# Kernel optimization log

Hardware: AMD Instinct MI355X
Metric: run time of the kernel (lower is better)

## Reference

```python
import jax, jax.numpy as jnp
import numpy as np
from jax import lax

C_IN, C_OUT, K = 32, 32, 3
DIV = float(np.sqrt(C_IN * K * K))  # sqrt(channels_in * filter_size^2)


def setup_inputs() -> dict:
    key = jax.random.key(0)
    kx, kw = jax.random.split(key)
    x = jax.random.normal(kx, (32, C_IN, 256, 256), dtype=jnp.float32)  # NCHW
    # torch.normal(0.0, 0.01, (Cout, Cin, k, k))
    weight = 0.01 * jax.random.normal(kw, (C_OUT, C_IN, K, K), dtype=jnp.float32)
    return {"x": x, "weight": weight}


def reference(x, weight):
    # binarize weights: sign with 0 -> -1 (torch.where(x > 0, 1.0, -1.0))
    weight_bin = jnp.where(weight > 0, 1.0, -1.0).astype(weight.dtype)
    # conv2d with 'same' padding (padding = k // 2, stride 1)
    out = lax.conv_general_dilated(
        x, weight_bin,
        window_strides=(1, 1),
        padding=((K // 2, K // 2), (K // 2, K // 2)),
        dimension_numbers=("NCHW", "OIHW", "NCHW"),
    )
    return out / DIV
```

## Files before the change

### kernel.cpp

```cpp
#include <hip/hip_runtime.h>


typedef __attribute__((ext_vector_type(8))) short short8;
typedef __attribute__((ext_vector_type(4))) float f32x4;

__device__ __forceinline__ unsigned short f2bf(float f) {
    unsigned int u = __builtin_bit_cast(unsigned int, f);
    u += 0x7FFFu + ((u >> 16) & 1u);
    return (unsigned short)(u >> 16);
}

__device__ __forceinline__ int lds_idx(int s, int p, int u) {
    return s * 264 + p * 4 + (u ^ ((p >> 1) & 3));
}

__global__ __launch_bounds__(512, 4)
void bconv2d_kernel(const float* __restrict__ x, const float* __restrict__ wgt,
                    float* __restrict__ out) {
    __shared__ short8 lds[8 * 264];

    const int tid = threadIdx.x;
    const int gx0 = blockIdx.x * 64;
    const int Y0  = blockIdx.y * 64;
    const int n   = blockIdx.z;

    const int l      = tid & 63;
    const int wv     = tid >> 6;
    const int r      = wv & 3;
    const int ch     = wv >> 2;
    const int lane15 = l & 15;
    const int lhi    = l >> 4;

    short8 afrag[3][3];
    {
        const int co  = ch * 16 + lane15;
        const int ci0 = lhi * 8;
        #pragma unroll
        for (int dy = 0; dy < 3; ++dy) {
            #pragma unroll
            for (int dx = 0; dx < 3; ++dx) {
                short8 a;
                #pragma unroll
                for (int j = 0; j < 8; ++j) {
                    float wval = wgt[((co * 32 + (ci0 + j)) * 3 + dy) * 3 + dx];
                    a[j] = (short)((wval > 0.0f) ? 0x3F80 : 0xBF80);
                }
                afrag[dy][dx] = a;
            }
        }
    }

    auto stage = [&](int gy0v, int nrows) {
        const int ntask = nrows * 264;
        for (int task = tid; task < ntask; task += 512) {
            const int row = task / 264;
            const int rem = task - row * 264;
            const int u   = rem / 66;
            const int p   = rem - u * 66;
            const int gy  = gy0v + row;
            const int gx  = gx0 - 1 + p;
            short8 v = (short8)0;
            if ((unsigned)gy < 256u && (unsigned)gx < 256u) {
                const float* src = x + (((size_t)n * 32 + u * 8) * 256 + gy) * 256 + gx;
                #pragma unroll
                for (int j = 0; j < 8; ++j)
                    v[j] = (short)f2bf(src[(size_t)j * 65536]);
            }
            lds[lds_idx(gy & 7, p, u)] = v;
        }
    };

    stage(Y0 - 1, 6);
    __syncthreads();

    const float invdiv = 0.05892556509887896f;

    for (int i = 0; i < 16; ++i) {
        const int Y = Y0 + 4 * i;
        const int y = Y + r;

        f32x4 acc[4];
        #pragma unroll
        for (int tp = 0; tp < 4; ++tp) acc[tp] = (f32x4)0.0f;

        #pragma unroll
        for (int dy = 0; dy < 3; ++dy) {
            const int sbase = ((y - 1 + dy) & 7) * 264;
            #pragma unroll
            for (int dx = 0; dx < 3; ++dx) {
                #pragma unroll
                for (int tp = 0; tp < 4; ++tp) {
                    const int p = tp * 16 + lane15 + dx;
                    short8 b = lds[sbase + p * 4 + (lhi ^ ((p >> 1) & 3))];
                    acc[tp] = __builtin_amdgcn_mfma_f32_16x16x32_bf16(
                        afrag[dy][dx], b, acc[tp], 0, 0, 0);
                }
            }
        }

        #pragma unroll
        for (int tp = 0; tp < 4; ++tp) {
            #pragma unroll
            for (int rr = 0; rr < 4; ++rr) {
                const int co = ch * 16 + lhi * 4 + rr;
                out[(((size_t)n * 32 + co) * 256 + y) * 256 + gx0 + tp * 16 + lane15]
                    = acc[tp][rr] * invdiv;
            }
        }

        __syncthreads();
        if (i < 15) stage(Y + 5, 4);
        __syncthreads();
    }
}

extern "C" void kernel_launch(void* const* d_in, const int* in_sizes, int n_in,
                              void* d_out, int out_size, void* d_ws, size_t ws_size,
                              hipStream_t stream) {
    const float* x   = (const float*)d_in[0];
    const float* wgt = (const float*)d_in[1];
    float* out = (float*)d_out;
    dim3 grid(4, 4, 32);
    dim3 block(512);
    bconv2d_kernel<<<grid, block, 0, stream>>>(x, wgt, out);
}
```

Baseline: 139.3 us.

## Split rows into 8-row blocks with two-row register blocking per wave

Each block now handles 8 output rows instead of 64, so the grid grows eightfold. Each block stages a 10-row halo once and no longer runs a sliding-window loop with per-iteration barriers. Each wave computes two adjacent output rows and reuses each LDS B fragment for both rows' MFMAs. The cost is a larger halo re-read (10 rows loaded per 8 outputs instead of 66 per 64) and a higher occupancy target in the launch bounds.

After: 305.8 us. 120% more time.

```diff
diff --git a/kernel.cpp b/kernel.cpp
--- a/kernel.cpp
+++ b/kernel.cpp
@@ -10,23 +10,19 @@
     return (unsigned short)(u >> 16);
 }
 
-__device__ __forceinline__ int lds_idx(int s, int p, int u) {
-    return s * 264 + p * 4 + (u ^ ((p >> 1) & 3));
-}
-
-__global__ __launch_bounds__(512, 4)
+__global__ __launch_bounds__(512, 6)
 void bconv2d_kernel(const float* __restrict__ x, const float* __restrict__ wgt,
                     float* __restrict__ out) {
-    __shared__ short8 lds[8 * 264];
+    __shared__ short8 lds[10 * 264];
 
     const int tid = threadIdx.x;
     const int gx0 = blockIdx.x * 64;
-    const int Y0  = blockIdx.y * 64;
+    const int Y0  = blockIdx.y * 8;
     const int n   = blockIdx.z;
 
     const int l      = tid & 63;
     const int wv     = tid >> 6;
-    const int r      = wv & 3;
+    const int rp     = (wv & 3) * 2;
     const int ch     = wv >> 2;
     const int lane15 = l & 15;
     const int lhi    = l >> 4;
@@ -50,67 +46,62 @@
         }
     }
 
-    auto stage = [&](int gy0v, int nrows) {
-        const int ntask = nrows * 264;
-        for (int task = tid; task < ntask; task += 512) {
-            const int row = task / 264;
-            const int rem = task - row * 264;
-            const int u   = rem / 66;
-            const int p   = rem - u * 66;
-            const int gy  = gy0v + row;
-            const int gx  = gx0 - 1 + p;
-            short8 v = (short8)0;
-            if ((unsigned)gy < 256u && (unsigned)gx < 256u) {
-                const float* src = x + (((size_t)n * 32 + u * 8) * 256 + gy) * 256 + gx;
-                #pragma unroll
-                for (int j = 0; j < 8; ++j)
-                    v[j] = (short)f2bf(src[(size_t)j * 65536]);
-            }
-            lds[lds_idx(gy & 7, p, u)] = v;
+    for (int task = tid; task < 10 * 264; task += 512) {
+        const int row = task / 264;
+        const int rem = task - row * 264;
+        const int u   = rem / 66;
+        const int p   = rem - u * 66;
+        const int gy  = Y0 - 1 + row;
+        const int gx  = gx0 - 1 + p;
+        short8 v = (short8)0;
+        if ((unsigned)gy < 256u && (unsigned)gx < 256u) {
+            const float* src = x + (((size_t)n * 32 + u * 8) * 256 + gy) * 256 + gx;
+            #pragma unroll
+            for (int j = 0; j < 8; ++j)
+                v[j] = (short)f2bf(src[(size_t)j * 65536]);
         }
-    };
-
-    stage(Y0 - 1, 6);
+        lds[row * 264 + p * 4 + (u ^ ((p >> 1) & 3))] = v;
+    }
     __syncthreads();
 
-    const float invdiv = 0.05892556509887896f;
+    f32x4 acc[2][4];
+    #pragma unroll
+    for (int rr = 0; rr < 2; ++rr)
+        #pragma unroll
+        for (int tp = 0; tp < 4; ++tp) acc[rr][tp] = (f32x4)0.0f;
 
-    for (int i = 0; i < 16; ++i) {
-        const int Y = Y0 + 4 * i;
-        const int y = Y + r;
-
-        f32x4 acc[4];
+    #pragma unroll
+    for (int ss = 0; ss < 4; ++ss) {
+        const int sbase = (rp + ss) * 264;
         #pragma unroll
-        for (int tp = 0; tp < 4; ++tp) acc[tp] = (f32x4)0.0f;
-
-        #pragma unroll
-        for (int dy = 0; dy < 3; ++dy) {
-            const int sbase = ((y - 1 + dy) & 7) * 264;
+        for (int dx = 0; dx < 3; ++dx) {
             #pragma unroll
-            for (int dx = 0; dx < 3; ++dx) {
-                #pragma unroll
-                for (int tp = 0; tp < 4; ++tp) {
-                    const int p = tp * 16 + lane15 + dx;
-                    short8 b = lds[sbase + p * 4 + (lhi ^ ((p >> 1) & 3))];
-                    acc[tp] = __builtin_amdgcn_mfma_f32_16x16x32_bf16(
-                        afrag[dy][dx], b, acc[tp], 0, 0, 0);
-                }
+            for (int tp = 0; tp < 4; ++tp) {
+                const int p = tp * 16 + lane15 + dx;
+                short8 b = lds[sbase + p * 4 + (lhi ^ ((p >> 1) & 3))];
+                if (ss < 3)
+                    acc[0][tp] = __builtin_amdgcn_mfma_f32_16x16x32_bf16(
+                        afrag[ss][dx], b, acc[0][tp], 0, 0, 0);
+                if (ss >= 1)
+                    acc[1][tp] = __builtin_amdgcn_mfma_f32_16x16x32_bf16(
+                        afrag[ss - 1][dx], b, acc[1][tp], 0, 0, 0);
             }
         }
+    }
 
+    const float invdiv = 0.05892556509887896f;
+    #pragma unroll
+    for (int rr = 0; rr < 2; ++rr) {
+        const int y = Y0 + rp + rr;
         #pragma unroll
         for (int tp = 0; tp < 4; ++tp) {
             #pragma unroll
-            for (int rr = 0; rr < 4; ++rr) {
-                const int co = ch * 16 + lhi * 4 + rr;
+            for (int q = 0; q < 4; ++q) {
+                const int co = ch * 16 + lhi * 4 + q;
                 out[(((size_t)n * 32 + co) * 256 + y) * 256 + gx0 + tp * 16 + lane15]
-                    = acc[tp][rr] * invdiv;
+                    = acc[rr][tp][q] * invdiv;
             }
         }
-
-        __syncthreads();
-        if (i < 15) stage(Y + 5, 4);
-        __syncthreads();
     }
 }
 
@@ -120,7 +111,7 @@
     const float* x   = (const float*)d_in[0];
     const float* wgt = (const float*)d_in[1];
     float* out = (float*)d_out;
-    dim3 grid(4, 4, 32);
+    dim3 grid(4, 32, 32);
     dim3 block(512);
     bconv2d_kernel<<<grid, block, 0, stream>>>(x, wgt, out);
 }
```

## Vectorize input staging, halve row tile, drop LDS swizzle, overlap stores with staging

Applied to the files above, without the earlier changes.

The staging loop now loads four consecutive floats per thread with 16-byte vector loads for the interior columns and handles the two halo columns separately, replacing scalar per-pixel loads. The LDS layout changes from an XOR-swizzled index to a plain linear one. Each block now covers 32 rows instead of 64 (twice as many blocks) and the launch-bounds occupancy hint rises to 6. Output stores are moved after the next stage is issued so global writes overlap the staging work. Risks are LDS bank conflicts from the unswizzled layout, extra halo reloads from smaller row tiles, and register pressure under the higher occupancy hint.

After: 274.5 us. 1.97x slower.

```diff
diff --git a/kernel.cpp b/kernel.cpp
--- a/kernel.cpp
+++ b/kernel.cpp
@@ -1,27 +1,24 @@
 #include <hip/hip_runtime.h>
+#include <hip/hip_bf16.h>
 
 
 typedef __attribute__((ext_vector_type(8))) short short8;
 typedef __attribute__((ext_vector_type(4))) float f32x4;
 
-__device__ __forceinline__ unsigned short f2bf(float f) {
+__device__ __forceinline__ short bf16s(float f) {
     unsigned int u = __builtin_bit_cast(unsigned int, f);
     u += 0x7FFFu + ((u >> 16) & 1u);
-    return (unsigned short)(u >> 16);
+    return (short)(u >> 16);
 }
 
-__device__ __forceinline__ int lds_idx(int s, int p, int u) {
-    return s * 264 + p * 4 + (u ^ ((p >> 1) & 3));
-}
-
-__global__ __launch_bounds__(512, 4)
+__global__ __launch_bounds__(512, 6)
 void bconv2d_kernel(const float* __restrict__ x, const float* __restrict__ wgt,
                     float* __restrict__ out) {
     __shared__ short8 lds[8 * 264];
 
     const int tid = threadIdx.x;
     const int gx0 = blockIdx.x * 64;
-    const int Y0  = blockIdx.y * 64;
+    const int Y0  = blockIdx.y * 32;
     const int n   = blockIdx.z;
 
     const int l      = tid & 63;
@@ -36,37 +33,60 @@
         const int co  = ch * 16 + lane15;
         const int ci0 = lhi * 8;
         #pragma unroll
-        for (int dy = 0; dy < 3; ++dy) {
+        for (int dy = 0; dy < 3; ++dy)
             #pragma unroll
             for (int dx = 0; dx < 3; ++dx) {
                 short8 a;
                 #pragma unroll
                 for (int j = 0; j < 8; ++j) {
-                    float wval = wgt[((co * 32 + (ci0 + j)) * 3 + dy) * 3 + dx];
+                    float wval = wgt[((co * 32 + ci0 + j) * 3 + dy) * 3 + dx];
                     a[j] = (short)((wval > 0.0f) ? 0x3F80 : 0xBF80);
                 }
                 afrag[dy][dx] = a;
             }
-        }
     }
 
+    const float* xn = x + (size_t)n * 32 * 65536;
+
     auto stage = [&](int gy0v, int nrows) {
-        const int ntask = nrows * 264;
-        for (int task = tid; task < ntask; task += 512) {
-            const int row = task / 264;
-            const int rem = task - row * 264;
-            const int u   = rem / 66;
-            const int p   = rem - u * 66;
-            const int gy  = gy0v + row;
-            const int gx  = gx0 - 1 + p;
-            short8 v = (short8)0;
-            if ((unsigned)gy < 256u && (unsigned)gx < 256u) {
-                const float* src = x + (((size_t)n * 32 + u * 8) * 256 + gy) * 256 + gx;
+        const int nq = nrows * 64;
+        const int nt = nq + nrows * 8;
+        for (int task = tid; task < nt; task += 512) {
+            if (task < nq) {
+                const int row = task >> 6;
+                const int u   = (task >> 4) & 3;
+                const int q   = task & 15;
+                const int gy  = gy0v + row;
+                short8 w[4] = {};
+                if ((unsigned)gy < 256u) {
+                    const float* src = xn + ((size_t)(u * 8) * 256 + gy) * 256 + gx0 + q * 4;
+                    #pragma unroll
+                    for (int j = 0; j < 8; ++j) {
+                        f32x4 v = *(const f32x4*)(src + (size_t)j * 65536);
+                        #pragma unroll
+                        for (int t = 0; t < 4; ++t)
+                            w[t][j] = bf16s(v[t]);
+                    }
+                }
+                const int base = (gy & 7) * 264 + u * 66 + q * 4 + 1;
                 #pragma unroll
-                for (int j = 0; j < 8; ++j)
-                    v[j] = (short)f2bf(src[(size_t)j * 65536]);
+                for (int t = 0; t < 4; ++t) lds[base + t] = w[t];
+            } else {
+                const int e    = task - nq;
+                const int row  = e >> 3;
+                const int u    = (e & 7) >> 1;
+                const int side = e & 1;
+                const int gy   = gy0v + row;
+                const int p    = side ? 65 : 0;
+                const int gx   = gx0 - 1 + p;
+                short8 w = {};
+                if ((unsigned)gy < 256u && (unsigned)gx < 256u) {
+                    const float* src = xn + ((size_t)(u * 8) * 256 + gy) * 256 + gx;
+                    #pragma unroll
+                    for (int j = 0; j < 8; ++j) w[j] = bf16s(src[(size_t)j * 65536]);
+                }
+                lds[(gy & 7) * 264 + u * 66 + p] = w;
             }
-            lds[lds_idx(gy & 7, p, u)] = v;
         }
     };
 
@@ -75,7 +95,7 @@
 
     const float invdiv = 0.05892556509887896f;
 
-    for (int i = 0; i < 16; ++i) {
+    for (int i = 0; i < 8; ++i) {
         const int Y = Y0 + 4 * i;
         const int y = Y + r;
 
@@ -84,32 +104,29 @@
         for (int tp = 0; tp < 4; ++tp) acc[tp] = (f32x4)0.0f;
 
         #pragma unroll
-        for (int dy = 0; dy < 3; ++dy) {
-            const int sbase = ((y - 1 + dy) & 7) * 264;
+        for (int ss = 0; ss < 3; ++ss) {
+            const int sbase = ((y - 1 + ss) & 7) * 264 + lhi * 66 + lane15;
             #pragma unroll
-            for (int dx = 0; dx < 3; ++dx) {
+            for (int dx = 0; dx < 3; ++dx)
                 #pragma unroll
                 for (int tp = 0; tp < 4; ++tp) {
-                    const int p = tp * 16 + lane15 + dx;
-                    short8 b = lds[sbase + p * 4 + (lhi ^ ((p >> 1) & 3))];
+                    short8 b = lds[sbase + tp * 16 + dx];
                     acc[tp] = __builtin_amdgcn_mfma_f32_16x16x32_bf16(
-                        afrag[dy][dx], b, acc[tp], 0, 0, 0);
+                        afrag[ss][dx], b, acc[tp], 0, 0, 0);
                 }
-            }
-        }
-
-        #pragma unroll
-        for (int tp = 0; tp < 4; ++tp) {
-            #pragma unroll
-            for (int rr = 0; rr < 4; ++rr) {
-                const int co = ch * 16 + lhi * 4 + rr;
-                out[(((size_t)n * 32 + co) * 256 + y) * 256 + gx0 + tp * 16 + lane15]
-                    = acc[tp][rr] * invdiv;
-            }
         }
 
         __syncthreads();
-        if (i < 15) stage(Y + 5, 4);
+        if (i < 7) stage(Y + 5, 4);
+
+        #pragma unroll
+        for (int tp = 0; tp < 4; ++tp)
+            #pragma unroll
+            for (int q = 0; q < 4; ++q) {
+                const int co = ch * 16 + lhi * 4 + q;
+                out[(((size_t)n * 32 + co) * 256 + y) * 256 + gx0 + tp * 16 + lane15]
+                    = acc[tp][q] * invdiv;
+            }
         __syncthreads();
     }
 }
@@ -120,7 +137,7 @@
     const float* x   = (const float*)d_in[0];
     const float* wgt = (const float*)d_in[1];
     float* out = (float*)d_out;
-    dim3 grid(4, 4, 32);
+    dim3 grid(4, 8, 32);
     dim3 block(512);
     bconv2d_kernel<<<grid, block, 0, stream>>>(x, wgt, out);
 }
```
